# Kernel tuning notes

Hardware: AMD Instinct MI355X
Metric: run time of the kernel (lower is better)

The kernel has to match this reference:

```python
import jax, jax.numpy as jnp
import numpy as np

D_MODEL = 1024
HEADS = 16
D_K = 64
B, S = 2, 2048


def setup_inputs() -> dict:
    key = jax.random.key(0)
    ks = jax.random.split(key, 12)
    s = 0.02
    return {
        "query": jax.random.normal(ks[0], (B, S, D_MODEL), dtype=jnp.float32),
        "key": jax.random.normal(ks[1], (B, S, D_MODEL), dtype=jnp.float32),
        "value": jax.random.normal(ks[2], (B, S, D_MODEL), dtype=jnp.float32),
        "Wq": jax.random.normal(ks[3], (D_MODEL, HEADS * D_K), dtype=jnp.float32) * s,
        "bq": jnp.zeros((HEADS * D_K,), dtype=jnp.float32),
        "Wk": jax.random.normal(ks[4], (D_MODEL, HEADS * D_K), dtype=jnp.float32) * s,
        "bk": jnp.zeros((HEADS * D_K,), dtype=jnp.float32),
        "Wv": jax.random.normal(ks[5], (D_MODEL, HEADS * D_K), dtype=jnp.float32) * s,
        "bv": jnp.zeros((HEADS * D_K,), dtype=jnp.float32),
        "Wo": jax.random.normal(ks[6], (HEADS * D_K, D_MODEL), dtype=jnp.float32) * s,
        "bo": jnp.zeros((D_MODEL,), dtype=jnp.float32),
    }


def reference(query, key, value, Wq, bq, Wk, bk, Wv, bv, Wo, bo):
    b, s, _ = query.shape
    scale = 1.0 / np.sqrt(D_K).astype(np.float32)
    # project and split heads: [b, s, h, d_k]
    q = (query @ Wq + bq).reshape(b, s, HEADS, D_K)
    k = (key @ Wk + bk).reshape(b, s, HEADS, D_K)
    v = (value @ Wv + bv).reshape(b, s, HEADS, D_K)
    # attention scores [b, i, j, h]
    scores = jnp.einsum('bihd,bjhd->bijh', q, k) * scale
    # NOTE: original uses nn.Softmax(dim=1) -> normalize over query axis i (faithful quirk)
    attn = jax.nn.softmax(scores, axis=1)
    # dropout is identity in eval mode
    x = jnp.einsum('bijh,bjhd->bihd', attn, v).reshape(b, s, HEADS * D_K)
    return x @ Wo + bo
```

## Files before the change

### kernel.cpp

```cpp
#include <hip/hip_runtime.h>
#include <hip/hip_bf16.h>

#define SEQ   2048
#define NH    16
#define DK    64
#define DM    1024
#define NTOK  4096
#define C1    0.1803368801111204f

typedef unsigned short u16;
typedef unsigned int   u32;
typedef short bhalf8 __attribute__((ext_vector_type(8)));
typedef float floatx4 __attribute__((ext_vector_type(4)));

#define MFMA16(a,b,c) __builtin_amdgcn_mfma_f32_16x16x32_bf16(a,b,c,0,0,0)

#if __has_builtin(__builtin_amdgcn_exp2f)
#define EXP2(x) __builtin_amdgcn_exp2f(x)
#else
#define EXP2(x) exp2f(x)
#endif

__device__ __forceinline__ u16 f2b(float f){
  union { float f; u32 u; } v; v.f = f;
  u32 r = v.u + 0x7fffu + ((v.u >> 16) & 1u);
  return (u16)(r >> 16);
}
__device__ __forceinline__ u32 pk2(float a, float b){
  union { __hip_bfloat162 h; u32 w; } o;
  o.h = __float22bfloat162_rn(make_float2(a, b));
  return o.w;
}
__device__ __forceinline__ void gld_lds16(const u16* g, u16* lds){
  __builtin_amdgcn_global_load_lds(
      (const __attribute__((address_space(1))) u32*)g,
      (__attribute__((address_space(3))) u32*)lds, 16, 0, 0);
}

__global__ __launch_bounds__(256)
void cvt_qkv(const float* __restrict__ q, const float* __restrict__ k,
             const float* __restrict__ v, u16* __restrict__ Aq,
             u16* __restrict__ Ak, u16* __restrict__ Av)
{
  const float* in = (blockIdx.y == 0) ? q : (blockIdx.y == 1) ? k : v;
  u16* out       = (blockIdx.y == 0) ? Aq : (blockIdx.y == 1) ? Ak : Av;
  const size_t i = ((size_t)blockIdx.x * 256 + threadIdx.x) * 8;
  const float4 a = *(const float4*)(in + i);
  const float4 b = *(const float4*)(in + i + 4);
  uint4 o;
  o.x = pk2(a.x, a.y); o.y = pk2(a.z, a.w);
  o.z = pk2(b.x, b.y); o.w = pk2(b.z, b.w);
  *(uint4*)(out + i) = o;
}

__global__ __launch_bounds__(256)
void wtrans4(const float* __restrict__ Wq, const float* __restrict__ Wk,
             const float* __restrict__ Wv, const float* __restrict__ Wo,
             u16* __restrict__ Wtall)
{
  __shared__ __align__(16) u16 T[64][68];
  const int z = blockIdx.z;
  const float* W = (z == 0) ? Wq : (z == 1) ? Wk : (z == 2) ? Wv : Wo;
  u16* Wt = Wtall + (size_t)z * DM * DM;
  const int k0 = blockIdx.y * 64, n0 = blockIdx.x * 64;
  const int t = threadIdx.x;
  #pragma unroll
  for (int p = 0; p < 16; ++p){
    int e = p*256 + t, k = e >> 6, n = e & 63;
    T[n][k] = f2b(W[(size_t)(k0+k)*DM + n0 + n]);
  }
  __syncthreads();
  #pragma unroll
  for (int p = 0; p < 8; ++p){
    int e = p*256 + t, n = e >> 5, kp = e & 31;
    u32 val = *(const u32*)&T[n][2*kp];
    *(u32*)&Wt[(size_t)(n0+n)*DM + k0 + 2*kp] = val;
  }
}

__global__ __launch_bounds__(256)
void gemm_qkv(const u16* __restrict__ Aq, const u16* __restrict__ Ak,
              const u16* __restrict__ Av, const u16* __restrict__ Wtall,
              const float* __restrict__ bq, const float* __restrict__ bk,
              const float* __restrict__ bv, u16* __restrict__ Qb,
              u16* __restrict__ Kb, u16* __restrict__ Vt)
{
  __shared__ __align__(16) u16 Asm[128*32];
  __shared__ __align__(16) u16 Bsm[128*32];
  const int z = blockIdx.z;
  const u16* A = (z == 0) ? Aq : (z == 1) ? Ak : Av;
  const u16* Wt = Wtall + (size_t)z * DM * DM;
  const float* bias = (z == 0) ? bq : (z == 1) ? bk : bv;
  const float cmul = (z == 0) ? C1 : 1.0f;

  const int bm = blockIdx.y * 128, bn = blockIdx.x * 128;
  const int t = threadIdx.x, wid = t >> 6, l = t & 63, r16 = l & 15, q = l >> 4;
  const int wm = (wid & 1) * 64, wn = (wid >> 1) * 64;
  const int rL = t >> 2, gL = ((t & 3) ^ (rL & 3)) * 8;
  const u16* Ag = A  + (size_t)(bm + rL)*DM + gL;
  const u16* Bg = Wt + (size_t)(bn + rL)*DM + gL;
  u16* AsmW = Asm + wid*512;
  u16* BsmW = Bsm + wid*512;
  const int sw = (r16 & 3);
  floatx4 acc[4][4] = {};

  for (int kc = 0; kc < DM; kc += 32){
    gld_lds16(Ag + kc,                 AsmW);
    gld_lds16(Ag + kc + (size_t)64*DM, AsmW + 2048);
    gld_lds16(Bg + kc,                 BsmW);
    gld_lds16(Bg + kc + (size_t)64*DM, BsmW + 2048);
    __syncthreads();
    bhalf8 af[4], bf[4];
    #pragma unroll
    for (int i = 0; i < 4; ++i)
      af[i] = *(const bhalf8*)&Asm[(wm + i*16 + r16)*32 + ((q ^ sw)*8)];
    #pragma unroll
    for (int j = 0; j < 4; ++j)
      bf[j] = *(const bhalf8*)&Bsm[(wn + j*16 + r16)*32 + ((q ^ sw)*8)];
    #pragma unroll
    for (int i = 0; i < 4; ++i)
      #pragma unroll
      for (int j = 0; j < 4; ++j)
        acc[i][j] = MFMA16(af[i], bf[j], acc[i][j]);
    __syncthreads();
  }

  if (z < 2){
    u16* C = (z == 0) ? Qb : Kb;
    #pragma unroll
    for (int j = 0; j < 4; ++j){
      const int n = bn + wn + j*16 + r16;
      const float bj = bias[n];
      #pragma unroll
      for (int i = 0; i < 4; ++i){
        const int m0 = bm + wm + i*16 + q*4;
        #pragma unroll
        for (int r = 0; r < 4; ++r)
          C[(size_t)(m0+r)*DM + n] = f2b((acc[i][j][r] + bj) * cmul);
      }
    }
  } else {
    const int h  = (bn + wn) >> 6;
    const int bb = (bm + wm) >> 11;
    const int s0 = (bm + wm) & (SEQ - 1);
    #pragma unroll
    for (int i = 0; i < 4; ++i){
      const int sl = s0 + i*16 + q*4;
      #pragma unroll
      for (int j = 0; j < 4; ++j){
        const int d = j*16 + r16;
        const float bj = bias[h*DK + d];
        u32 v0 = pk2(acc[i][j][0]+bj, acc[i][j][1]+bj);
        u32 v1 = pk2(acc[i][j][2]+bj, acc[i][j][3]+bj);
        *(uint2*)&Vt[((size_t)(bb*NH + h)*DK + d)*SEQ + sl] = make_uint2(v0, v1);
      }
    }
  }
}

__global__ __launch_bounds__(256)
void gemm_o(const u16* __restrict__ A, const u16* __restrict__ Wt,
            const float* __restrict__ bias, float* __restrict__ C)
{
  __shared__ __align__(16) u16 Asm[128*32];
  __shared__ __align__(16) u16 Bsm[128*32];
  const int bm = blockIdx.y * 128, bn = blockIdx.x * 128;
  const int t = threadIdx.x, wid = t >> 6, l = t & 63, r16 = l & 15, q = l >> 4;
  const int wm = (wid & 1) * 64, wn = (wid >> 1) * 64;
  const int rL = t >> 2, gL = ((t & 3) ^ (rL & 3)) * 8;
  const u16* Ag = A  + (size_t)(bm + rL)*DM + gL;
  const u16* Bg = Wt + (size_t)(bn + rL)*DM + gL;
  u16* AsmW = Asm + wid*512;
  u16* BsmW = Bsm + wid*512;
  const int sw = (r16 & 3);
  floatx4 acc[4][4] = {};

  for (int kc = 0; kc < DM; kc += 32){
    gld_lds16(Ag + kc,                 AsmW);
    gld_lds16(Ag + kc + (size_t)64*DM, AsmW + 2048);
    gld_lds16(Bg + kc,                 BsmW);
    gld_lds16(Bg + kc + (size_t)64*DM, BsmW + 2048);
    __syncthreads();
    bhalf8 af[4], bf[4];
    #pragma unroll
    for (int i = 0; i < 4; ++i)
      af[i] = *(const bhalf8*)&Asm[(wm + i*16 + r16)*32 + ((q ^ sw)*8)];
    #pragma unroll
    for (int j = 0; j < 4; ++j)
      bf[j] = *(const bhalf8*)&Bsm[(wn + j*16 + r16)*32 + ((q ^ sw)*8)];
    #pragma unroll
    for (int i = 0; i < 4; ++i)
      #pragma unroll
      for (int j = 0; j < 4; ++j)
        acc[i][j] = MFMA16(af[i], bf[j], acc[i][j]);
    __syncthreads();
  }
  #pragma unroll
  for (int j = 0; j < 4; ++j){
    const int n = bn + wn + j*16 + r16;
    const float bj = bias[n];
    #pragma unroll
    for (int i = 0; i < 4; ++i){
      const int m0 = bm + wm + i*16 + q*4;
      #pragma unroll
      for (int r = 0; r < 4; ++r)
        C[(size_t)(m0+r)*DM + n] = acc[i][j][r] + bj;
    }
  }
}

__global__ __launch_bounds__(256)
void attn_stats(const u16* __restrict__ Qb, const u16* __restrict__ Kb,
                u16* __restrict__ Vt)
{
  __shared__ float pl[4][64];
  __shared__ float sLinv[64];
  const int j0 = blockIdx.x * 64, bh = blockIdx.y, b = bh >> 4, h = bh & 15;
  const int t = threadIdx.x, wid = t >> 6, l = t & 63, r16 = l & 15, q = l >> 4;

  bhalf8 kf[4][2];
  const u16* kp = Kb + (size_t)(b*SEQ + j0 + r16)*DM + h*DK + q*8;
  #pragma unroll
  for (int st = 0; st < 4; ++st){
    kf[st][0] = *(const bhalf8*)(kp + (size_t)st*16*DM);
    kf[st][1] = *(const bhalf8*)(kp + (size_t)st*16*DM + 32);
  }
  float rl[4] = {0.f, 0.f, 0.f, 0.f};
  const u16* qp = Qb + (size_t)(b*SEQ + wid*16 + r16)*DM + h*DK + q*8;
  for (int it = 0; it < SEQ/64; ++it){
    bhalf8 qf0 = *(const bhalf8*)qp;
    bhalf8 qf1 = *(const bhalf8*)(qp + 32);
    qp += (size_t)64*DM;
    #pragma unroll
    for (int st = 0; st < 4; ++st){
      floatx4 s = {};
      s = MFMA16(qf0, kf[st][0], s);
      s = MFMA16(qf1, kf[st][1], s);
      rl[st] += EXP2(s[0]) + EXP2(s[1]) + EXP2(s[2]) + EXP2(s[3]);
    }
  }
  #pragma unroll
  for (int st = 0; st < 4; ++st){
    float v = rl[st];
    v += __shfl_xor(v, 16);
    v += __shfl_xor(v, 32);
    rl[st] = v;
  }
  if (q == 0){
    #pragma unroll
    for (int st = 0; st < 4; ++st) pl[wid][st*16 + r16] = rl[st];
  }
  __syncthreads();
  if (t < 64)
    sLinv[t] = 1.f / (pl[0][t] + pl[1][t] + pl[2][t] + pl[3][t]);
  __syncthreads();
  {
    const int d = t >> 2, cb = (t & 3) * 16;
    u16* vp = Vt + ((size_t)bh*DK + d)*SEQ + j0 + cb;
    uint4 w0 = *(uint4*)vp, w1 = *(uint4*)(vp + 8);
    float sc[16];
    #pragma unroll
    for (int e = 0; e < 16; ++e) sc[e] = sLinv[cb + e];
    #define SC2(w, s0, s1) pk2(__uint_as_float((w) << 16) * (s0), \
                               __uint_as_float((w) & 0xffff0000u) * (s1))
    w0.x = SC2(w0.x, sc[0],  sc[1]);  w0.y = SC2(w0.y, sc[2],  sc[3]);
    w0.z = SC2(w0.z, sc[4],  sc[5]);  w0.w = SC2(w0.w, sc[6],  sc[7]);
    w1.x = SC2(w1.x, sc[8],  sc[9]);  w1.y = SC2(w1.y, sc[10], sc[11]);
    w1.z = SC2(w1.z, sc[12], sc[13]); w1.w = SC2(w1.w, sc[14], sc[15]);
    #undef SC2
    *(uint4*)vp = w0; *(uint4*)(vp + 8) = w1;
  }
}

__global__ __launch_bounds__(256)
void attn_pv(const u16* __restrict__ Qb, const u16* __restrict__ Kb,
             const u16* __restrict__ Vt, u16* __restrict__ Xb)
{
  __shared__ __align__(16) u16 Kls[64*64];
  __shared__ __align__(16) u16 Vls[64*64];
  __shared__ __align__(16) u16 Pls[4][32][72];
  const int i0 = blockIdx.x * 128, bh = blockIdx.y, b = bh >> 4, h = bh & 15;
  const int t = threadIdx.x, wid = t >> 6, l = t & 63, r16 = l & 15, q = l >> 4;

  bhalf8 qf[2][2];
  #pragma unroll
  for (int g = 0; g < 2; ++g){
    const u16* qp = Qb + (size_t)(b*SEQ + i0 + wid*32 + g*16 + r16)*DM + h*DK + q*8;
    qf[g][0] = *(const bhalf8*)qp;
    qf[g][1] = *(const bhalf8*)(qp + 32);
  }

  const int row0 = t >> 3, c0 = t & 7;
  const int g0 = (c0 ^ (row0 & 7)) * 8;
  const int row1 = row0 + 32;
  const int g1 = (c0 ^ (row1 & 7)) * 8;
  const u16* kp0 = Kb + (size_t)(b*SEQ + row0)*DM + h*DK + g0;
  const u16* kp1 = Kb + (size_t)(b*SEQ + row1)*DM + h*DK + g1;
  const u16* vp0 = Vt + ((size_t)bh*DK + row0)*SEQ + g0;
  const u16* vp1 = Vt + ((size_t)bh*DK + row1)*SEQ + g1;
  u16* kdst = Kls + wid*512;
  u16* vdst = Vls + wid*512;
  const int sw = (r16 & 7);

  floatx4 xacc[2][4] = {};
  for (int jt = 0; jt < SEQ/64; ++jt){
    gld_lds16(kp0 + (size_t)jt*64*DM, kdst);
    gld_lds16(kp1 + (size_t)jt*64*DM, kdst + 2048);
    gld_lds16(vp0 + jt*64,            vdst);
    gld_lds16(vp1 + jt*64,            vdst + 2048);
    __syncthreads();

    #pragma unroll
    for (int st = 0; st < 4; ++st){
      const int kr = (st*16 + r16) * 64;
      bhalf8 k0 = *(const bhalf8*)&Kls[kr + ((q     ^ sw) * 8)];
      bhalf8 k1 = *(const bhalf8*)&Kls[kr + (((q+4) ^ sw) * 8)];
      #pragma unroll
      for (int g = 0; g < 2; ++g){
        floatx4 s = {};
        s = MFMA16(k0, qf[g][0], s);
        s = MFMA16(k1, qf[g][1], s);
        u32 lo = pk2(EXP2(s[0]), EXP2(s[1]));
        u32 hi = pk2(EXP2(s[2]), EXP2(s[3]));
        *(uint2*)&Pls[wid][g*16 + r16][st*16 + q*4] = make_uint2(lo, hi);
      }
    }
    #pragma unroll
    for (int g = 0; g < 2; ++g){
      bhalf8 pf0 = *(const bhalf8*)&Pls[wid][g*16 + r16][q*8];
      bhalf8 pf1 = *(const bhalf8*)&Pls[wid][g*16 + r16][32 + q*8];
      #pragma unroll
      for (int dst = 0; dst < 4; ++dst){
        const int vr = (dst*16 + r16) * 64;
        bhalf8 v0 = *(const bhalf8*)&Vls[vr + ((q     ^ sw) * 8)];
        bhalf8 v1 = *(const bhalf8*)&Vls[vr + (((q+4) ^ sw) * 8)];
        xacc[g][dst] = MFMA16(pf0, v0, xacc[g][dst]);
        xacc[g][dst] = MFMA16(pf1, v1, xacc[g][dst]);
      }
    }
    __syncthreads();
  }

  #pragma unroll
  for (int g = 0; g < 2; ++g)
    #pragma unroll
    for (int dst = 0; dst < 4; ++dst)
      #pragma unroll
      for (int r = 0; r < 4; ++r)
        Xb[(size_t)(b*SEQ + i0 + wid*32 + g*16 + q*4 + r)*DM + h*DK + dst*16 + r16]
          = f2b(xacc[g][dst][r]);
}

extern "C" void kernel_launch(void* const* d_in, const int* in_sizes, int n_in,
                              void* d_out, int out_size, void* d_ws, size_t ws_size,
                              hipStream_t stream)
{
  const float* q  = (const float*)d_in[0];
  const float* k  = (const float*)d_in[1];
  const float* v  = (const float*)d_in[2];
  const float* Wq = (const float*)d_in[3];
  const float* bq = (const float*)d_in[4];
  const float* Wk = (const float*)d_in[5];
  const float* bk = (const float*)d_in[6];
  const float* Wv = (const float*)d_in[7];
  const float* bv = (const float*)d_in[8];
  const float* Wo = (const float*)d_in[9];
  const float* bo = (const float*)d_in[10];
  float* out = (float*)d_out;

  char* ws = (char*)d_ws;
  const size_t WTB  = (size_t)DM * DM * sizeof(u16);
  const size_t TOKB = (size_t)NTOK * DM * sizeof(u16);
  u16* Wtall = (u16*)(ws);
  u16* Aq    = (u16*)(ws + 4*WTB);
  u16* Ak    = (u16*)(ws + 4*WTB + TOKB);
  u16* Av    = (u16*)(ws + 4*WTB + 2*TOKB);
  u16* Qb    = (u16*)(ws + 4*WTB + 3*TOKB);
  u16* Kb    = (u16*)(ws + 4*WTB + 4*TOKB);
  u16* Vt    = (u16*)(ws + 4*WTB + 5*TOKB);
  u16* Xb    = Aq;

  dim3 blk(256);
  cvt_qkv<<<dim3((NTOK*DM)/(256*8), 3), blk, 0, stream>>>(q, k, v, Aq, Ak, Av);
  wtrans4<<<dim3(16, 16, 4), blk, 0, stream>>>(Wq, Wk, Wv, Wo, Wtall);
  gemm_qkv<<<dim3(DM/128, NTOK/128, 3), blk, 0, stream>>>(
      Aq, Ak, Av, Wtall, bq, bk, bv, Qb, Kb, Vt);
  attn_stats<<<dim3(SEQ/64, NH*2), blk, 0, stream>>>(Qb, Kb, Vt);
  attn_pv<<<dim3(SEQ/128, NH*2), blk, 0, stream>>>(Qb, Kb, Vt, Xb);
  gemm_o<<<dim3(DM/128, NTOK/128), blk, 0, stream>>>(
      Xb, Wtall + 3*(size_t)DM*DM, bo, out);
}
```

Baseline: 288.7 us.

## Double-buffer K/V tiles in LDS and prefetch the next tile during compute

The attention kernel now keeps two LDS buffers each for the K and V tiles. It issues the global-to-LDS loads for tile jt+1 before computing on tile jt, which drops one barrier per iteration and overlaps load latency with the MFMA and exp work. V fragments are read into registers at the start of each iteration, and the compute section is wrapped in s_setprio to favour it. In exchange, LDS use per block roughly doubles for K/V, which may lower occupancy, and the hoisted V fragments raise register pressure.

```diff
diff --git a/kernel.cpp b/kernel.cpp
--- a/kernel.cpp
+++ b/kernel.cpp
@@ -276,8 +276,8 @@
 void attn_pv(const u16* __restrict__ Qb, const u16* __restrict__ Kb,
              const u16* __restrict__ Vt, u16* __restrict__ Xb)
 {
-  __shared__ __align__(16) u16 Kls[64*64];
-  __shared__ __align__(16) u16 Vls[64*64];
+  __shared__ __align__(16) u16 Kls[2][64*64];
+  __shared__ __align__(16) u16 Vls[2][64*64];
   __shared__ __align__(16) u16 Pls[4][32][72];
   const int i0 = blockIdx.x * 128, bh = blockIdx.y, b = bh >> 4, h = bh & 15;
   const int t = threadIdx.x, wid = t >> 6, l = t & 63, r16 = l & 15, q = l >> 4;
@@ -298,23 +298,43 @@
   const u16* kp1 = Kb + (size_t)(b*SEQ + row1)*DM + h*DK + g1;
   const u16* vp0 = Vt + ((size_t)bh*DK + row0)*SEQ + g0;
   const u16* vp1 = Vt + ((size_t)bh*DK + row1)*SEQ + g1;
-  u16* kdst = Kls + wid*512;
-  u16* vdst = Vls + wid*512;
+  const int wo = wid*512;
   const int sw = (r16 & 7);
 
   floatx4 xacc[2][4] = {};
+
+  gld_lds16(kp0, &Kls[0][wo]);
+  gld_lds16(kp1, &Kls[0][wo + 2048]);
+  gld_lds16(vp0, &Vls[0][wo]);
+  gld_lds16(vp1, &Vls[0][wo + 2048]);
+  __syncthreads();
+
+  int cur = 0;
   for (int jt = 0; jt < SEQ/64; ++jt){
-    gld_lds16(kp0 + (size_t)jt*64*DM, kdst);
-    gld_lds16(kp1 + (size_t)jt*64*DM, kdst + 2048);
-    gld_lds16(vp0 + jt*64,            vdst);
-    gld_lds16(vp1 + jt*64,            vdst + 2048);
-    __syncthreads();
+    if (jt + 1 < SEQ/64){
+      const int nx = cur ^ 1;
+      gld_lds16(kp0 + (size_t)(jt+1)*64*DM, &Kls[nx][wo]);
+      gld_lds16(kp1 + (size_t)(jt+1)*64*DM, &Kls[nx][wo + 2048]);
+      gld_lds16(vp0 + (jt+1)*64,            &Vls[nx][wo]);
+      gld_lds16(vp1 + (jt+1)*64,            &Vls[nx][wo + 2048]);
+    }
+    const u16* Kc = &Kls[cur][0];
+    const u16* Vc = &Vls[cur][0];
+
+    __builtin_amdgcn_s_setprio(1);
+    bhalf8 vf[4][2];
+    #pragma unroll
+    for (int dst = 0; dst < 4; ++dst){
+      const int vr = (dst*16 + r16) * 64;
+      vf[dst][0] = *(const bhalf8*)&Vc[vr + ((q     ^ sw) * 8)];
+      vf[dst][1] = *(const bhalf8*)&Vc[vr + (((q+4) ^ sw) * 8)];
+    }
 
     #pragma unroll
     for (int st = 0; st < 4; ++st){
       const int kr = (st*16 + r16) * 64;
-      bhalf8 k0 = *(const bhalf8*)&Kls[kr + ((q     ^ sw) * 8)];
-      bhalf8 k1 = *(const bhalf8*)&Kls[kr + (((q+4) ^ sw) * 8)];
+      bhalf8 k0 = *(const bhalf8*)&Kc[kr + ((q     ^ sw) * 8)];
+      bhalf8 k1 = *(const bhalf8*)&Kc[kr + (((q+4) ^ sw) * 8)];
       #pragma unroll
       for (int g = 0; g < 2; ++g){
         floatx4 s = {};
@@ -331,14 +351,13 @@
       bhalf8 pf1 = *(const bhalf8*)&Pls[wid][g*16 + r16][32 + q*8];
       #pragma unroll
       for (int dst = 0; dst < 4; ++dst){
-        const int vr = (dst*16 + r16) * 64;
-        bhalf8 v0 = *(const bhalf8*)&Vls[vr + ((q     ^ sw) * 8)];
-        bhalf8 v1 = *(const bhalf8*)&Vls[vr + (((q+4) ^ sw) * 8)];
-        xacc[g][dst] = MFMA16(pf0, v0, xacc[g][dst]);
-        xacc[g][dst] = MFMA16(pf1, v1, xacc[g][dst]);
+        xacc[g][dst] = MFMA16(pf0, vf[dst][0], xacc[g][dst]);
+        xacc[g][dst] = MFMA16(pf1, vf[dst][1], xacc[g][dst]);
       }
     }
+    __builtin_amdgcn_s_setprio(0);
     __syncthreads();
+    cur ^= 1;
   }
 
   #pragma unroll
```

New measurement: 280.0 us. 3.0% less time.
